# Kernel tuning notes

Measured on AMD Instinct MI355X. Metric: run time of the kernel, lower is better.

## Reference

```python
import jax, jax.numpy as jnp
import numpy as np

B, N, OBS, ACT = 128, 32, 64, 16
D = OBS + ACT       # obs_z_input_dim = 80
H = 64              # hardcoded hidden width
WOUT = 64           # weight_output_dim (d_k_weight)
ZOUT = 64           # obs_z_output_dim (d_k_obsz)
FIN = OBS + ZOUT    # final_input_dim = 128
FOUT = 1            # final_output_dim


def _lin_params(key, fan_in, fan_out):
    k1, k2 = jax.random.split(key)
    w = jax.random.normal(k1, (fan_in, fan_out), jnp.float32) / np.sqrt(fan_in).astype(np.float32)
    b = jax.random.normal(k2, (fan_out,), jnp.float32) * 0.01
    return w, b


def setup_inputs() -> dict:
    key = jax.random.key(0)
    ks = jax.random.split(key, 16)
    inp = {
        "states": jax.random.normal(ks[0], (B, N, OBS), jnp.float32),
        "policies": jax.random.uniform(ks[1], (B, N, ACT), jnp.float32),
        "actions": jax.random.uniform(ks[2], (B, N, ACT), jnp.float32),
    }
    specs = [("kw", OBS, WOUT), ("qw", OBS, WOUT), ("ko", D, ZOUT),
             ("qo", D, ZOUT), ("av", D, ZOUT), ("fv", FIN, FOUT)]
    for idx, (nm, din, dout) in enumerate(specs):
        w1, b1 = _lin_params(ks[3 + 2 * idx], din, H)
        w2, b2 = _lin_params(ks[4 + 2 * idx], H, dout)
        inp[nm + "1_w"], inp[nm + "1_b"] = w1, b1
        inp[nm + "2_w"], inp[nm + "2_b"] = w2, b2
    return inp


def _mlp(x, w1, b1, w2, b2):
    return jax.nn.leaky_relu(x @ w1 + b1) @ w2 + b2


def reference(states, policies, actions,
              kw1_w, kw1_b, kw2_w, kw2_b,
              qw1_w, qw1_b, qw2_w, qw2_b,
              ko1_w, ko1_b, ko2_w, ko2_b,
              qo1_w, qo1_b, qo2_w, qo2_b,
              av1_w, av1_b, av2_w, av2_b,
              fv1_w, fv1_b, fv2_w, fv2_b):
    # --- mixing weight between taken actions and policies ---
    key_z = _mlp(states, kw1_w, kw1_b, kw2_w, kw2_b)    # [B,N,WOUT]
    query_z = _mlp(states, qw1_w, qw1_b, qw2_w, qw2_b)  # [B,N,WOUT]
    # torch: bmm(q, k^T).transpose(1,2) => weight_z[b,a,j] = sigmoid(q[b,j].k[b,a]/sqrt(dk))
    scores_z = jnp.einsum('bad,bjd->baj', key_z, query_z)
    weight_z = jax.nn.sigmoid(scores_z / np.float32(np.sqrt(WOUT)))[..., None]  # [B,N,N,1]

    # z[b,a,j] = w[b,a,j]*actions[b,j] + (1-w)*policies[b,j]
    z = weight_z * actions[:, None, :, :] + (1.0 - weight_z) * policies[:, None, :, :]  # [B,N,N,ACT]
    states_b = jnp.broadcast_to(states[:, None, :, :], (B, N, N, OBS))  # states_rep[b,a,j]=states[b,j]
    obs_z = jnp.concatenate([states_b, z], axis=-1)                     # [B,N,N,D]

    # source_obsz one-hot-diag trick selects obs_z[b,a,a] (broadcast over j)
    diag = jnp.arange(N)
    source = obs_z[:, diag, diag, :]                                    # [B,N,D]
    key_obsz = _mlp(source, ko1_w, ko1_b, ko2_w, ko2_b)                 # [B,N,ZOUT]
    query_obsz = _mlp(obs_z, qo1_w, qo1_b, qo2_w, qo2_b)                # [B,N,N,ZOUT]
    scores_obsz = jnp.sum(key_obsz[:, :, None, :] * query_obsz, axis=-1)  # [B,N,N]
    weight_obsz = jax.nn.softmax(scores_obsz / np.float32(np.sqrt(ZOUT)), axis=-1)
    ret_weight_obsz = weight_obsz[..., None]                            # [B,N,N,1]

    # obs_z_pi[b,a,k,j] = cat(states[b,j], policies[b,j]) if j==k else obs_z[b,a,j]
    # (place_zs / place_policies masking). The attention-value MLP is pointwise
    # over the last dim, so apply it to the two distinct branches and combine:
    vals = _mlp(obs_z, av1_w, av1_b, av2_w, av2_b)                      # [B,N,N,ZOUT]
    sp = jnp.concatenate([states, policies], axis=-1)                   # [B,N,D]
    vals_pi = _mlp(sp, av1_w, av1_b, av2_w, av2_b)                      # [B,N,ZOUT]

    w = weight_obsz  # broadcast weight w5[b,a,k,j] = w[b,a,j]
    sum_all = jnp.einsum('baj,bajd->bad', w, vals)                      # [B,N,ZOUT]
    node_features = (sum_all[:, :, None, :]
                     - w[..., None] * vals
                     + w[..., None] * vals_pi[:, None, :, :]) / N       # [B,N,N,ZOUT]

    node_in = jnp.concatenate([states_b, node_features], axis=-1)       # [B,N,N,FIN]
    value = _mlp(node_in, fv1_w, fv1_b, fv2_w, fv2_b)                   # [B,N,N,1]
    return value, weight_z, ret_weight_obsz
```

## Files before the change

### kernel.cpp

```cpp
#include <hip/hip_runtime.h>

#define NN   32
#define HID  64

typedef __attribute__((ext_vector_type(8))) short bf16x8;
typedef __attribute__((ext_vector_type(4))) float f32x4;
typedef unsigned short u16;
typedef unsigned int   u32;

__device__ __forceinline__ float leaky(float v) { return v >= 0.f ? v : 0.01f * v; }
__device__ __forceinline__ float wsum64(float p) {
#pragma unroll
    for (int o = 32; o; o >>= 1) p += __shfl_xor(p, o);
    return p;
}
__device__ __forceinline__ u16 f2bf(float f) {
    union { float f; u32 u; } v; v.f = f;
    return (u16)((v.u + 0x7FFFu + ((v.u >> 16) & 1)) >> 16);
}
__device__ __forceinline__ float bf2f(short s) {
    union { u32 u; float f; } v; v.u = ((u32)(u16)s) << 16;
    return v.f;
}
__device__ __forceinline__ bf16x8 pack8(const float* v) {
    bf16x8 r;
#pragma unroll
    for (int e = 0; e < 8; ++e) r[e] = (short)f2bf(v[e]);
    return r;
}
__device__ __forceinline__ int swz(int row, int col)   { return row * 64 + ((((col >> 3) ^ (row & 7)) << 3) | (col & 7)); }
__device__ __forceinline__ int swz32(int row, int col) { return row * 32 + ((((col >> 3) ^ (row & 3)) << 3) | (col & 7)); }

__device__ __forceinline__ f32x4 gemm64(f32x4 C, const u16* A, const u16* W, int lm, int kb8, int bcol) {
#pragma unroll
    for (int k0 = 0; k0 < 64; k0 += 32) {
        const int g = (k0 >> 3) + kb8;
        const bf16x8 a = *(const bf16x8*)&A[lm * 64 + ((g ^ (lm & 7)) << 3)];
        const bf16x8 w = *(const bf16x8*)&W[bcol * 64 + ((g ^ (bcol & 7)) << 3)];
        C = __builtin_amdgcn_mfma_f32_16x16x32_bf16(a, w, C, 0, 0, 0);
    }
    return C;
}
__device__ __forceinline__ f32x4 gemm32(f32x4 C, const u16* A, const u16* W, int lm, int kb8, int bcol) {
    const bf16x8 a = *(const bf16x8*)&A[lm * 32 + ((kb8 ^ (lm & 3)) << 3)];
    const bf16x8 w = *(const bf16x8*)&W[bcol * 32 + ((kb8 ^ (bcol & 3)) << 3)];
    return __builtin_amdgcn_mfma_f32_16x16x32_bf16(a, w, C, 0, 0, 0);
}

#define W_KW1  0
#define W_KW2  4096
#define W_QW1  8192
#define W_QW2  12288
#define W_KO1A 16384
#define W_KO2  20480
#define W_QO2  24576
#define W_QO1A 28672
#define W_AV1A 32768
#define W_FV1A 36864
#define W_KO1B 40960
#define W_QO1B 43008
#define W_AV1B 45056

__global__ __launch_bounds__(256)
void prep_kernel(const float* __restrict__ av2_w, const float* __restrict__ av2_b,
                 const float* __restrict__ fv1_w,
                 const float* __restrict__ kw1_w, const float* __restrict__ kw2_w,
                 const float* __restrict__ qw1_w, const float* __restrict__ qw2_w,
                 const float* __restrict__ ko1_w, const float* __restrict__ ko2_w,
                 const float* __restrict__ qo2_w, const float* __restrict__ qo1_w,
                 const float* __restrict__ av1_w,
                 u16* __restrict__ MT, float* __restrict__ c, u16* __restrict__ wt)
{
    const int blk = blockIdx.x, t = threadIdx.x;
    if (blk == 0) {
        const int h = t & 63, jg = t >> 6;
        __shared__ float sA[4096];
        for (int i = t; i < 4096; i += 256) sA[i] = av2_w[i];
        __syncthreads();
        const float* W = fv1_w + 4096;
        float acc[16];
#pragma unroll
        for (int i = 0; i < 16; ++i) acc[i] = 0.f;
        for (int m = 0; m < 64; ++m) {
            const float w = W[m * 64 + h];
#pragma unroll
            for (int i = 0; i < 16; ++i)
                acc[i] = fmaf(sA[(jg + 4 * i) * 64 + m], w, acc[i]);
        }
#pragma unroll
        for (int i = 0; i < 16; ++i) { const int k = jg + 4 * i; MT[swz(h, k)] = f2bf(acc[i]); }
        if (t < 64) {
            float s = 0.f;
            for (int m = 0; m < 64; ++m) s = fmaf(av2_b[m], W[m * 64 + t], s);
            c[t] = s;
        }
    } else if (blk <= 9) {
        const float* srcs[9] = {kw1_w, kw2_w, qw1_w, qw2_w, ko1_w, ko2_w, qo1_w, av1_w, fv1_w};
        const int    offs[9] = {W_KW1, W_KW2, W_QW1, W_QW2, W_KO1A, W_KO2, W_QO1A, W_AV1A, W_FV1A};
        const float* W = srcs[blk - 1]; u16* dst = wt + offs[blk - 1];
        for (int i = t; i < 4096; i += 256) { const int k = i >> 6, h = i & 63; dst[swz(h, k)] = f2bf(W[i]); }
    } else if (blk == 10) {
        u16* dst = wt + W_QO2;
        for (int i = t; i < 4096; i += 256) { const int h = i >> 6, d = i & 63; dst[swz(h, d)] = f2bf(qo2_w[i]); }
    } else if (blk <= 13) {
        const float* srcs[3] = {ko1_w + 4096, qo1_w + 4096, av1_w + 4096};
        const int    offs[3] = {W_KO1B, W_QO1B, W_AV1B};
        const float* W = srcs[blk - 11]; u16* dst = wt + offs[blk - 11];
        for (int i = t; i < 1024; i += 256) {
            const int k = i >> 6, h = i & 63;
            dst[swz32(h, k)]      = f2bf(W[i]);
            dst[swz32(h, 16 + k)] = 0;
        }
    }
}

__global__ __launch_bounds__(256)
void setup_kernel(const float* __restrict__ states, const float* __restrict__ policies,
                  const float* __restrict__ actions,
                  const float* __restrict__ kw1_b, const float* __restrict__ kw2_b,
                  const float* __restrict__ qw1_b, const float* __restrict__ qw2_b,
                  const float* __restrict__ ko1_b, const float* __restrict__ ko2_b,
                  const float* __restrict__ qo1_b, const float* __restrict__ qo2_b,
                  const float* __restrict__ av1_b, const float* __restrict__ fv1_b,
                  const u16* __restrict__ wt, const u16* __restrict__ MT,
                  const float* __restrict__ c_,
                  u32* __restrict__ kzg, u32* __restrict__ qzg,
                  float* __restrict__ kq, float* __restrict__ kb,
                  float* __restrict__ baseq, float* __restrict__ deltaq,
                  float* __restrict__ basev, float* __restrict__ deltav,
                  float* __restrict__ pre, float* __restrict__ vpf)
{
    const int blk = blockIdx.x;
    const int row0 = blk * 16;
    const int t = threadIdx.x, lane = t & 63, jg = t >> 6;
    const int lm = lane & 15, kb8 = lane >> 4, cg = jg * 16 + lm;

    __shared__ __align__(16) u16 aST[1024], aH1[1024], aH2[1024], aKZ[1024], aQZ[1024];
    __shared__ __align__(16) u16 aP2[512], aDAP[512];
    __shared__ float fACT[256], fPOL[256];
    __shared__ float fKOBS[16 * 68];
    __shared__ float wzd[16];

    {
        const int i = t * 4, row = i >> 6, col = i & 63;
        const float4 s4 = *(const float4*)&states[row0 * 64 + i];
        const int base = swz(row, col);
        aST[base + 0] = f2bf(s4.x); aST[base + 1] = f2bf(s4.y);
        aST[base + 2] = f2bf(s4.z); aST[base + 3] = f2bf(s4.w);
        const float av = actions[row0 * 16 + t], pv = policies[row0 * 16 + t];
        fACT[t] = av; fPOL[t] = pv;
        const int r2 = t >> 4, cc = t & 15;
        aDAP[swz32(r2, cc)]      = f2bf(av - pv);
        aDAP[swz32(r2, 16 + cc)] = 0;
        aP2 [swz32(r2, 16 + cc)] = 0;
    }
    __syncthreads();

    {
        f32x4 C = {0.f,0.f,0.f,0.f};
        C = gemm64(C, aST, wt + W_KW1, lm, kb8, cg);
        const float bv = kw1_b[cg];
#pragma unroll
        for (int rr = 0; rr < 4; ++rr) aH1[swz(kb8 * 4 + rr, cg)] = f2bf(leaky(C[rr] + bv));
    }
    __syncthreads();

    {
        f32x4 C = {0.f,0.f,0.f,0.f};
        C = gemm64(C, aH1, wt + W_KW2, lm, kb8, cg);
        const float bv = kw2_b[cg];
#pragma unroll
        for (int rr = 0; rr < 4; ++rr) aKZ[swz(kb8 * 4 + rr, cg)] = f2bf(C[rr] + bv);
        f32x4 D = {0.f,0.f,0.f,0.f};
        D = gemm64(D, aST, wt + W_QW1, lm, kb8, cg);
        const float bq = qw1_b[cg];
#pragma unroll
        for (int rr = 0; rr < 4; ++rr) aH2[swz(kb8 * 4 + rr, cg)] = f2bf(leaky(D[rr] + bq));
    }
    __syncthreads();

    {
        f32x4 C = {0.f,0.f,0.f,0.f};
        C = gemm64(C, aH2, wt + W_QW2, lm, kb8, cg);
        const float bv = qw2_b[cg];
#pragma unroll
        for (int rr = 0; rr < 4; ++rr) aQZ[swz(kb8 * 4 + rr, cg)] = f2bf(C[rr] + bv);
    }
    __syncthreads();

    if (jg == 0) {
        f32x4 C = {0.f,0.f,0.f,0.f};
#pragma unroll
        for (int k0 = 0; k0 < 64; k0 += 32) {
            const int g = (k0 >> 3) + kb8;
            const bf16x8 a  = *(const bf16x8*)&aKZ[lm * 64 + ((g ^ (lm & 7)) << 3)];
            const bf16x8 qb = *(const bf16x8*)&aQZ[lm * 64 + ((g ^ (lm & 7)) << 3)];
            C = __builtin_amdgcn_mfma_f32_16x16x32_bf16(a, qb, C, 0, 0, 0);
        }
        if ((lm >> 2) == kb8) wzd[lm] = 1.f / (1.f + __expf(-C[lm & 3] * 0.125f));
    } else if (jg == 1) {
        const u32* s = (const u32*)aKZ;
        for (int i = lane; i < 512; i += 64) kzg[blk * 512 + i] = s[i];
    } else if (jg == 2) {
        const u32* s = (const u32*)aQZ;
        for (int i = lane; i < 512; i += 64) qzg[blk * 512 + i] = s[i];
    }
    __syncthreads();

    {
        const int r2 = t >> 4, cc = t & 15;
        const float w = wzd[r2];
        aP2[swz32(r2, cc)] = f2bf(w * fACT[t] + (1.f - w) * fPOL[t]);
    }
    __syncthreads();

    {
        f32x4 C = {0.f,0.f,0.f,0.f};
        C = gemm64(C, aST, wt + W_KO1A, lm, kb8, cg);
        C = gemm32(C, aP2, wt + W_KO1B, lm, kb8, cg);
        const float bv = ko1_b[cg];
#pragma unroll
        for (int rr = 0; rr < 4; ++rr) aH1[swz(kb8 * 4 + rr, cg)] = f2bf(leaky(C[rr] + bv));
    }
    __syncthreads();

    {
        f32x4 C = {0.f,0.f,0.f,0.f};
        C = gemm64(C, aH1, wt + W_KO2, lm, kb8, cg);
        const float bv = ko2_b[cg];
#pragma unroll
        for (int rr = 0; rr < 4; ++rr) {
            const float v = C[rr] + bv;
            aH2[swz(kb8 * 4 + rr, cg)] = f2bf(v);
            fKOBS[(kb8 * 4 + rr) * 68 + cg] = v;
        }
        const int r2 = t >> 4, cc = t & 15;
        aP2[swz32(r2, cc)] = f2bf(fPOL[t]);
    }
    __syncthreads();

    {
        f32x4 C = {0.f,0.f,0.f,0.f};
        C = gemm64(C, aH2, wt + W_QO2, lm, kb8, cg);
#pragma unroll
        for (int rr = 0; rr < 4; ++rr) kq[(row0 + kb8 * 4 + rr) * 64 + cg] = C[rr] * 0.125f;
    }
    {
        const float qb = qo2_b[lane];
#pragma unroll
        for (int q = 0; q < 4; ++q) {
            const int r = jg * 4 + q;
            const float s = wsum64(qb * fKOBS[r * 68 + lane]);
            if (lane == 0) kb[row0 + r] = s * 0.125f;
        }
    }
    {
        f32x4 C = {0.f,0.f,0.f,0.f};
        C = gemm64(C, aST, wt + W_QO1A, lm, kb8, cg);
        C = gemm32(C, aP2, wt + W_QO1B, lm, kb8, cg);
        const float bv = qo1_b[cg];
#pragma unroll
        for (int rr = 0; rr < 4; ++rr) baseq[(row0 + kb8 * 4 + rr) * 64 + cg] = C[rr] + bv;
    }
    {
        f32x4 C = {0.f,0.f,0.f,0.f};
        C = gemm32(C, aDAP, wt + W_QO1B, lm, kb8, cg);
#pragma unroll
        for (int rr = 0; rr < 4; ++rr) deltaq[(row0 + kb8 * 4 + rr) * 64 + cg] = C[rr];
    }
    {
        f32x4 C = {0.f,0.f,0.f,0.f};
        C = gemm64(C, aST, wt + W_AV1A, lm, kb8, cg);
        C = gemm32(C, aP2, wt + W_AV1B, lm, kb8, cg);
        const float bv = av1_b[cg];
#pragma unroll
        for (int rr = 0; rr < 4; ++rr) {
            const float v = C[rr] + bv;
            basev[(row0 + kb8 * 4 + rr) * 64 + cg] = v;
            aH1[swz(kb8 * 4 + rr, cg)] = f2bf(leaky(v));
        }
    }
    {
        f32x4 C = {0.f,0.f,0.f,0.f};
        C = gemm32(C, aDAP, wt + W_AV1B, lm, kb8, cg);
#pragma unroll
        for (int rr = 0; rr < 4; ++rr) deltav[(row0 + kb8 * 4 + rr) * 64 + cg] = C[rr];
    }
    {
        f32x4 C = {0.f,0.f,0.f,0.f};
        C = gemm64(C, aST, wt + W_FV1A, lm, kb8, cg);
        const float bv = fv1_b[cg];
#pragma unroll
        for (int rr = 0; rr < 4; ++rr) pre[(row0 + kb8 * 4 + rr) * 64 + cg] = C[rr] + bv;
    }
    __syncthreads();

    {
        f32x4 C = {0.f,0.f,0.f,0.f};
        C = gemm64(C, aH1, MT, lm, kb8, cg);
        const float bv = c_[cg];
#pragma unroll
        for (int rr = 0; rr < 4; ++rr) vpf[(row0 + kb8 * 4 + rr) * 64 + cg] = C[rr] + bv;
    }
}

__global__ __launch_bounds__(256)
void main_kernel(const u32* __restrict__ kzg,   const u32* __restrict__ qzg,
                 const float* __restrict__ kq,  const float* __restrict__ kb,
                 const float* __restrict__ baseq, const float* __restrict__ deltaq,
                 const float* __restrict__ basev, const float* __restrict__ deltav,
                 const float* __restrict__ pre,   const float* __restrict__ vpf,
                 const u16* __restrict__ MT,
                 const float* __restrict__ c,
                 const float* __restrict__ fv2_w, const float* __restrict__ fv2_b,
                 float* __restrict__ out_value,
                 float* __restrict__ out_wz,
                 float* __restrict__ out_wobs)
{
    const int bid0 = blockIdx.x;
    const int bid  = (bid0 & 7) * 64 + (bid0 >> 3);
    const int b = bid >> 2, a0 = (bid & 3) * 8;
    const int t = threadIdx.x, lane = t & 63, jg = t >> 6;
    const int row = t >> 3, s8 = t & 7, c0 = s8 * 8;

    __shared__ __align__(16) u16 sMT[4096];
    __shared__ __align__(16) u16 sQZ[2048];
    __shared__ __align__(16) u16 sKZ8[512];
    __shared__ __align__(16) u16 sHV[2048];
    __shared__ float sKQ[512];
    __shared__ float sC[32 * 65];
    __shared__ float sHB[64];
    __shared__ float s_sc[32];
    __shared__ float skb[8];

    {
        u32* d = (u32*)sMT;  for (int i = t; i < 2048; i += 256) d[i] = ((const u32*)MT)[i];
        u32* q = (u32*)sQZ;  for (int i = t; i < 1024; i += 256) q[i] = qzg[b * 1024 + i];
        ((u32*)sKZ8)[t] = kzg[b * 1024 + a0 * 32 + t];
        for (int i = t; i < 512; i += 256) sKQ[i] = kq[(b * 32 + a0) * 64 + i];
        if (t < 8) skb[t] = kb[b * 32 + a0 + t];
    }
    const int rb = (b * 32 + row) * 64 + c0;
    const float4 q0 = *(const float4*)&baseq[rb],  q1 = *(const float4*)&baseq[rb + 4];
    const float4 d0 = *(const float4*)&deltaq[rb], d1 = *(const float4*)&deltaq[rb + 4];
    const float4 v0 = *(const float4*)&basev[rb],  v1 = *(const float4*)&basev[rb + 4];
    const float4 e0 = *(const float4*)&deltav[rb], e1 = *(const float4*)&deltav[rb + 4];
    const float4 p0 = *(const float4*)&pre[rb],    p1 = *(const float4*)&pre[rb + 4];
    const float4 f0 = *(const float4*)&vpf[rb],    f1 = *(const float4*)&vpf[rb + 4];
    const float4 cc0 = *(const float4*)&c[c0],     cc1 = *(const float4*)&c[c0 + 4];
    const float4 fw0 = *(const float4*)&fv2_w[c0], fw1 = *(const float4*)&fv2_w[c0 + 4];
    const float fb2 = fv2_b[0];
    const float bqL[8] = {q0.x,q0.y,q0.z,q0.w,q1.x,q1.y,q1.z,q1.w};
    const float dqL[8] = {d0.x,d0.y,d0.z,d0.w,d1.x,d1.y,d1.z,d1.w};
    const float bvL[8] = {v0.x,v0.y,v0.z,v0.w,v1.x,v1.y,v1.z,v1.w};
    const float dvL[8] = {e0.x,e0.y,e0.z,e0.w,e1.x,e1.y,e1.z,e1.w};
    const float preL[8] = {p0.x,p0.y,p0.z,p0.w,p1.x,p1.y,p1.z,p1.w};
    const float vpfL[8] = {f0.x,f0.y,f0.z,f0.w,f1.x,f1.y,f1.z,f1.w};
    const float cL[8]  = {cc0.x,cc0.y,cc0.z,cc0.w,cc1.x,cc1.y,cc1.z,cc1.w};
    const float fwL[8] = {fw0.x,fw0.y,fw0.z,fw0.w,fw1.x,fw1.y,fw1.z,fw1.w};
    __syncthreads();

    const int gq = s8 ^ (row & 7);

    for (int ai = 0; ai < 8; ++ai) {
        const int a = a0 + ai;

        float wzv;
        {
            const bf16x8 kzp = *(const bf16x8*)&sKZ8[ai * 64 + ((s8 ^ ai) << 3)];
            const bf16x8 qzp = *(const bf16x8*)&sQZ[row * 64 + (gq << 3)];
            float p = 0.f;
#pragma unroll
            for (int e = 0; e < 8; ++e)
                p = fmaf(bf2f(kzp[e]), bf2f(qzp[e]), p);
            p += __shfl_xor(p, 1); p += __shfl_xor(p, 2); p += __shfl_xor(p, 4);
            wzv = 1.f / (1.f + __expf(-p * 0.125f));
            if (s8 == 0) out_wz[b * 1024 + a * 32 + row] = wzv;
        }

        {
            float p = 0.f;
#pragma unroll
            for (int e = 0; e < 8; ++e)
                p = fmaf(leaky(bqL[e] + wzv * dqL[e]), sKQ[ai * 64 + c0 + e], p);
            p += __shfl_xor(p, 1); p += __shfl_xor(p, 2); p += __shfl_xor(p, 4);
            if (s8 == 0) s_sc[row] = p + skb[ai];
        }

        {
            float hv[8];
#pragma unroll
            for (int e = 0; e < 8; ++e) hv[e] = leaky(bvL[e] + wzv * dvL[e]);
            *(bf16x8*)&sHV[row * 64 + (gq << 3)] = pack8(hv);
        }
        __syncthreads();

        float wreg;
        {
            const float sreg = s_sc[lane & 31];
            float m = sreg;
#pragma unroll
            for (int o = 1; o < 32; o <<= 1) m = fmaxf(m, __shfl_xor(m, o));
            const float e = __expf(sreg - m);
            float ssum = e;
#pragma unroll
            for (int o = 1; o < 32; o <<= 1) ssum += __shfl_xor(ssum, o);
            wreg = e / ssum;
            if (t < 32) out_wobs[b * 1024 + a * 32 + t] = wreg;
        }

        {
            const int lm = lane & 15, kb8 = lane >> 4;
            const int bcol = jg * 16 + lm;
            f32x4 acc0 = {0.f,0.f,0.f,0.f}, acc1 = {0.f,0.f,0.f,0.f};
#pragma unroll
            for (int k0 = 0; k0 < 64; k0 += 32) {
                const int g = (k0 >> 3) + kb8;
                const bf16x8 bf = *(const bf16x8*)&sMT[bcol * 64 + ((g ^ (bcol & 7)) << 3)];
                const bf16x8 A0 = *(const bf16x8*)&sHV[lm * 64 + ((g ^ (lm & 7)) << 3)];
                const bf16x8 A1 = *(const bf16x8*)&sHV[(16 + lm) * 64 + ((g ^ (lm & 7)) << 3)];
                acc0 = __builtin_amdgcn_mfma_f32_16x16x32_bf16(A0, bf, acc0, 0, 0, 0);
                acc1 = __builtin_amdgcn_mfma_f32_16x16x32_bf16(A1, bf, acc1, 0, 0, 0);
            }
            float hb = 0.f;
#pragma unroll
            for (int rr = 0; rr < 4; ++rr) {
                const int r0 = kb8 * 4 + rr, r1 = 16 + r0;
                sC[r0 * 65 + bcol] = acc0[rr];
                sC[r1 * 65 + bcol] = acc1[rr];
                hb = fmaf(__shfl(wreg, r0), acc0[rr], hb);
                hb = fmaf(__shfl(wreg, r1), acc1[rr], hb);
            }
            hb += __shfl_xor(hb, 16);
            hb += __shfl_xor(hb, 32);
            if (lane < 16) sHB[bcol] = hb;
        }
        __syncthreads();

        {
            const float wrow = __shfl(wreg, row);
            float vpart = 0.f;
#pragma unroll
            for (int e = 0; e < 8; ++e) {
                const int col = c0 + e;
                float g = preL[e] + (sHB[col] - wrow * sC[row * 65 + col]
                                     + (1.f - wrow) * cL[e] + wrow * vpfL[e]) * (1.f / 32.f);
                vpart = fmaf(leaky(g), fwL[e], vpart);
            }
            vpart += __shfl_xor(vpart, 1); vpart += __shfl_xor(vpart, 2); vpart += __shfl_xor(vpart, 4);
            if (s8 == 0) out_value[b * 1024 + a * 32 + row] = vpart + fb2;
        }
    }
}

extern "C" void kernel_launch(void* const* d_in, const int* in_sizes, int n_in,
                              void* d_out, int out_size, void* d_ws, size_t ws_size,
                              hipStream_t stream)
{
    const float* states   = (const float*)d_in[0];
    const float* policies = (const float*)d_in[1];
    const float* actions  = (const float*)d_in[2];
    const float* kw1_w = (const float*)d_in[3];  const float* kw1_b = (const float*)d_in[4];
    const float* kw2_w = (const float*)d_in[5];  const float* kw2_b = (const float*)d_in[6];
    const float* qw1_w = (const float*)d_in[7];  const float* qw1_b = (const float*)d_in[8];
    const float* qw2_w = (const float*)d_in[9];  const float* qw2_b = (const float*)d_in[10];
    const float* ko1_w = (const float*)d_in[11]; const float* ko1_b = (const float*)d_in[12];
    const float* ko2_w = (const float*)d_in[13]; const float* ko2_b = (const float*)d_in[14];
    const float* qo1_w = (const float*)d_in[15]; const float* qo1_b = (const float*)d_in[16];
    const float* qo2_w = (const float*)d_in[17]; const float* qo2_b = (const float*)d_in[18];
    const float* av1_w = (const float*)d_in[19]; const float* av1_b = (const float*)d_in[20];
    const float* av2_w = (const float*)d_in[21]; const float* av2_b = (const float*)d_in[22];
    const float* fv1_w = (const float*)d_in[23]; const float* fv1_b = (const float*)d_in[24];
    const float* fv2_w = (const float*)d_in[25]; const float* fv2_b = (const float*)d_in[26];

    float* out       = (float*)d_out;
    float* out_value = out;
    float* out_wz    = out + 131072;
    float* out_wobs  = out + 262144;

    const int SZ = 262144;
    float* ws   = (float*)d_ws;
    float* c_   = ws;
    float* kb_  = ws + 64;
    u16*   MT_  = (u16*)(ws + 4160);
    u32*   kzg  = (u32*)(ws + 6208);
    u32*   qzg  = (u32*)(ws + 137280);
    float* kq_   = ws + 268352;
    float* baseq = kq_   + SZ;
    float* dq_   = baseq + SZ;
    float* basev = dq_   + SZ;
    float* dv_   = basev + SZ;
    float* pre_  = dv_   + SZ;
    float* vpf_  = pre_  + SZ;
    u16*   wt_   = (u16*)(ws + 2103360);

    prep_kernel<<<14, 256, 0, stream>>>(
        av2_w, av2_b, fv1_w,
        kw1_w, kw2_w, qw1_w, qw2_w, ko1_w, ko2_w, qo2_w, qo1_w, av1_w,
        MT_, c_, wt_);

    setup_kernel<<<256, 256, 0, stream>>>(
        states, policies, actions,
        kw1_b, kw2_b, qw1_b, qw2_b, ko1_b, ko2_b, qo1_b, qo2_b, av1_b, fv1_b,
        wt_, MT_, c_,
        kzg, qzg, kq_, kb_, baseq, dq_, basev, dv_, pre_, vpf_);

    main_kernel<<<512, 256, 0, stream>>>(
        kzg, qzg, kq_, kb_, baseq, dq_, basev, dv_, pre_, vpf_,
        MT_, c_, fv2_w, fv2_b,
        out_value, out_wz, out_wobs);
}
```

Baseline: 44.56 us.

## Split main kernel into 2048 blocks of two agents, drop shared staging

The main kernel now launches four times as many blocks, each handling two agent rows instead of eight, to raise parallelism and occupancy across the GPU. The shared-memory staging of MT, query/key embeddings and kq is removed: per-thread query data is read straight from global memory into registers, key and kq values are loaded per iteration, and the MFMA B operand is read directly from global MT. This cuts LDS footprint and the upfront sync, at the cost of redundant per-block global loads of base/delta/pre tensors that are now repeated by four times more blocks. Global reads for the MFMA operand rely on cache hits.

```diff
diff --git a/kernel.cpp b/kernel.cpp
--- a/kernel.cpp
+++ b/kernel.cpp
@@ -318,35 +318,23 @@
                  float* __restrict__ out_wobs)
 {
     const int bid0 = blockIdx.x;
-    const int bid  = (bid0 & 7) * 64 + (bid0 >> 3);
-    const int b = bid >> 2, a0 = (bid & 3) * 8;
+    const int bid  = (bid0 & 7) * 256 + (bid0 >> 3);
+    const int b = bid >> 4, a0 = (bid & 15) * 2;
     const int t = threadIdx.x, lane = t & 63, jg = t >> 6;
     const int row = t >> 3, s8 = t & 7, c0 = s8 * 8;
 
-    __shared__ __align__(16) u16 sMT[4096];
-    __shared__ __align__(16) u16 sQZ[2048];
-    __shared__ __align__(16) u16 sKZ8[512];
     __shared__ __align__(16) u16 sHV[2048];
-    __shared__ float sKQ[512];
     __shared__ float sC[32 * 65];
     __shared__ float sHB[64];
     __shared__ float s_sc[32];
-    __shared__ float skb[8];
-
-    {
-        u32* d = (u32*)sMT;  for (int i = t; i < 2048; i += 256) d[i] = ((const u32*)MT)[i];
-        u32* q = (u32*)sQZ;  for (int i = t; i < 1024; i += 256) q[i] = qzg[b * 1024 + i];
-        ((u32*)sKZ8)[t] = kzg[b * 1024 + a0 * 32 + t];
-        for (int i = t; i < 512; i += 256) sKQ[i] = kq[(b * 32 + a0) * 64 + i];
-        if (t < 8) skb[t] = kb[b * 32 + a0 + t];
-    }
-    const int rb = (b * 32 + row) * 64 + c0;
-    const float4 q0 = *(const float4*)&baseq[rb],  q1 = *(const float4*)&baseq[rb + 4];
-    const float4 d0 = *(const float4*)&deltaq[rb], d1 = *(const float4*)&deltaq[rb + 4];
-    const float4 v0 = *(const float4*)&basev[rb],  v1 = *(const float4*)&basev[rb + 4];
-    const float4 e0 = *(const float4*)&deltav[rb], e1 = *(const float4*)&deltav[rb + 4];
-    const float4 p0 = *(const float4*)&pre[rb],    p1 = *(const float4*)&pre[rb + 4];
-    const float4 f0 = *(const float4*)&vpf[rb],    f1 = *(const float4*)&vpf[rb + 4];
+
+    const int base = b * 2048 + t * 8;
+    const float4 q0 = *(const float4*)&baseq[base],  q1 = *(const float4*)&baseq[base + 4];
+    const float4 d0 = *(const float4*)&deltaq[base], d1 = *(const float4*)&deltaq[base + 4];
+    const float4 v0 = *(const float4*)&basev[base],  v1 = *(const float4*)&basev[base + 4];
+    const float4 e0 = *(const float4*)&deltav[base], e1 = *(const float4*)&deltav[base + 4];
+    const float4 p0 = *(const float4*)&pre[base],    p1 = *(const float4*)&pre[base + 4];
+    const float4 f0 = *(const float4*)&vpf[base],    f1 = *(const float4*)&vpf[base + 4];
     const float4 cc0 = *(const float4*)&c[c0],     cc1 = *(const float4*)&c[c0 + 4];
     const float4 fw0 = *(const float4*)&fv2_w[c0], fw1 = *(const float4*)&fv2_w[c0 + 4];
     const float fb2 = fv2_b[0];
@@ -358,40 +346,45 @@
     const float vpfL[8] = {f0.x,f0.y,f0.z,f0.w,f1.x,f1.y,f1.z,f1.w};
     const float cL[8]  = {cc0.x,cc0.y,cc0.z,cc0.w,cc1.x,cc1.y,cc1.z,cc1.w};
     const float fwL[8] = {fw0.x,fw0.y,fw0.z,fw0.w,fw1.x,fw1.y,fw1.z,fw1.w};
-    __syncthreads();
-
-    const int gq = s8 ^ (row & 7);
-
-    for (int ai = 0; ai < 8; ++ai) {
+    const int Gj = s8 ^ (row & 7);
+    const u32* qzt = qzg + ((b * 2 + (row >> 4)) << 9) + ((row & 15) << 5) + (Gj << 2);
+    const u32 qzu0 = qzt[0], qzu1 = qzt[1], qzu2 = qzt[2], qzu3 = qzt[3];
+
+    for (int ai = 0; ai < 2; ++ai) {
         const int a = a0 + ai;
 
         float wzv;
         {
-            const bf16x8 kzp = *(const bf16x8*)&sKZ8[ai * 64 + ((s8 ^ ai) << 3)];
-            const bf16x8 qzp = *(const bf16x8*)&sQZ[row * 64 + (gq << 3)];
+            const int Ga = s8 ^ (a & 7);
+            const u32* kzt = kzg + ((b * 2 + (a >> 4)) << 9) + ((a & 15) << 5) + (Ga << 2);
             float p = 0.f;
-#pragma unroll
-            for (int e = 0; e < 8; ++e)
-                p = fmaf(bf2f(kzp[e]), bf2f(qzp[e]), p);
+            const u32 qs[4] = {qzu0, qzu1, qzu2, qzu3};
+#pragma unroll
+            for (int e = 0; e < 4; ++e) {
+                const u32 ku = kzt[e], qu = qs[e];
+                p = fmaf(bf2f((short)(ku & 0xFFFF)), bf2f((short)(qu & 0xFFFF)), p);
+                p = fmaf(bf2f((short)(ku >> 16)),   bf2f((short)(qu >> 16)),   p);
+            }
             p += __shfl_xor(p, 1); p += __shfl_xor(p, 2); p += __shfl_xor(p, 4);
             wzv = 1.f / (1.f + __expf(-p * 0.125f));
             if (s8 == 0) out_wz[b * 1024 + a * 32 + row] = wzv;
         }
-
         {
+            const float4 k0 = *(const float4*)&kq[(b * 32 + a) * 64 + c0];
+            const float4 k1 = *(const float4*)&kq[(b * 32 + a) * 64 + c0 + 4];
+            const float kqL[8] = {k0.x,k0.y,k0.z,k0.w,k1.x,k1.y,k1.z,k1.w};
             float p = 0.f;
 #pragma unroll
             for (int e = 0; e < 8; ++e)
-                p = fmaf(leaky(bqL[e] + wzv * dqL[e]), sKQ[ai * 64 + c0 + e], p);
+                p = fmaf(leaky(bqL[e] + wzv * dqL[e]), kqL[e], p);
             p += __shfl_xor(p, 1); p += __shfl_xor(p, 2); p += __shfl_xor(p, 4);
-            if (s8 == 0) s_sc[row] = p + skb[ai];
-        }
-
+            if (s8 == 0) s_sc[row] = p + kb[b * 32 + a];
+        }
         {
             float hv[8];
 #pragma unroll
             for (int e = 0; e < 8; ++e) hv[e] = leaky(bvL[e] + wzv * dvL[e]);
-            *(bf16x8*)&sHV[row * 64 + (gq << 3)] = pack8(hv);
+            *(bf16x8*)&sHV[row * 64 + (Gj << 3)] = pack8(hv);
         }
         __syncthreads();
 
@@ -408,7 +401,6 @@
             wreg = e / ssum;
             if (t < 32) out_wobs[b * 1024 + a * 32 + t] = wreg;
         }
-
         {
             const int lm = lane & 15, kb8 = lane >> 4;
             const int bcol = jg * 16 + lm;
@@ -416,7 +408,7 @@
 #pragma unroll
             for (int k0 = 0; k0 < 64; k0 += 32) {
                 const int g = (k0 >> 3) + kb8;
-                const bf16x8 bf = *(const bf16x8*)&sMT[bcol * 64 + ((g ^ (bcol & 7)) << 3)];
+                const bf16x8 bf = *(const bf16x8*)&MT[bcol * 64 + ((g ^ (bcol & 7)) << 3)];
                 const bf16x8 A0 = *(const bf16x8*)&sHV[lm * 64 + ((g ^ (lm & 7)) << 3)];
                 const bf16x8 A1 = *(const bf16x8*)&sHV[(16 + lm) * 64 + ((g ^ (lm & 7)) << 3)];
                 acc0 = __builtin_amdgcn_mfma_f32_16x16x32_bf16(A0, bf, acc0, 0, 0, 0);
@@ -425,7 +417,7 @@
             float hb = 0.f;
 #pragma unroll
             for (int rr = 0; rr < 4; ++rr) {
-                const int r0 = kb8 * 4 + rr, r1 = 16 + r0;
+                const int r0 = kb8 * 4 + rr, r1 = 16 + kb8 * 4 + rr;
                 sC[r0 * 65 + bcol] = acc0[rr];
                 sC[r1 * 65 + bcol] = acc1[rr];
                 hb = fmaf(__shfl(wreg, r0), acc0[rr], hb);
@@ -505,7 +497,7 @@
         wt_, MT_, c_,
         kzg, qzg, kq_, kb_, baseq, dq_, basev, dv_, pre_, vpf_);
 
-    main_kernel<<<512, 256, 0, stream>>>(
+    main_kernel<<<2048, 256, 0, stream>>>(
         kzg, qzg, kq_, kb_, baseq, dq_, basev, dv_, pre_, vpf_,
         MT_, c_, fv2_w, fv2_b,
         out_value, out_wz, out_wobs);
```

New measurement: 43.18 us. 1.03x faster.
